# Kernel tuning notes

Measured on AMD Instinct MI355X. Metric: run time of the kernel, lower is better.

## Reference

```python
import jax, jax.numpy as jnp
import numpy as np

B, D = 8192, 1024          # batch, input dim
UNITS = [1024, 512]        # expert MLP hidden sizes
T, E_T, E_S = 2, 2, 4      # num_tasks, experts per task, shared experts
E = T * E_T + E_S          # total experts = 8


def setup_inputs() -> dict:
    key = jax.random.key(0)
    k = jax.random.split(key, 6)
    H, O = UNITS
    x = jax.random.normal(k[0], (B, D), dtype=jnp.float32)
    # glorot-normal-ish scaling for expert weights
    W1 = jax.random.normal(k[1], (E, D, H), dtype=jnp.float32) * np.sqrt(2.0 / (D + H))
    b1 = jnp.zeros((E, H), dtype=jnp.float32)
    W2 = jax.random.normal(k[2], (E, H, O), dtype=jnp.float32) * np.sqrt(2.0 / (H + O))
    b2 = jnp.zeros((E, O), dtype=jnp.float32)
    # per-task gate over (E_T + E_S) experts, no bias (use_bias=False in Dense)
    Wg = jax.random.normal(k[3], (T, D, E_T + E_S), dtype=jnp.float32) * np.sqrt(2.0 / (D + E_T + E_S))
    # shared gate over all E experts
    Wgs = jax.random.normal(k[4], (D, E), dtype=jnp.float32) * np.sqrt(2.0 / (D + E))
    return {"x": x, "W1": W1, "b1": b1, "W2": W2, "b2": b2, "Wg": Wg, "Wgs": Wgs}


def reference(x, W1, b1, W2, b2, Wg, Wgs):
    # All experts see the same input (2D-input path of CGC3: tf.tile over experts).
    # Batched grouped GEMM over the expert axis instead of a Python loop.
    h = jax.nn.relu(jnp.einsum('bd,edh->ebh', x, W1) + b1[:, None, :])   # [E,B,H]
    eo = jax.nn.relu(jnp.einsum('ebh,eho->ebo', h, W2) + b2[:, None, :]) # [E,B,O]

    outs = []
    for i in range(T):
        # experts for task i = its own E_T experts + the last E_S shared experts
        idx = jnp.array(list(range(i * E_T, (i + 1) * E_T)) + list(range(E - E_S, E)))
        g = jax.nn.softmax(x @ Wg[i], axis=-1)            # [B, E_T+E_S]
        sel = eo[idx]                                     # [E_T+E_S, B, O]
        outs.append(jnp.einsum('be,ebo->bo', g, sel))     # [B, O]
    # output_share=True: share tower gated over all experts
    gs = jax.nn.softmax(x @ Wgs, axis=-1)                 # [B, E]
    outs.append(jnp.einsum('be,ebo->bo', gs, eo))         # [B, O]
    return jnp.stack(outs, axis=1)                        # [B, T+1, O]
```

## Files before the change

kernel.cpp:

```cpp
#include <hip/hip_runtime.h>
#include <hip/hip_bf16.h>
#include <stdint.h>

#define B_SZ 8192
#define D_SZ 1024
#define H_SZ 1024
#define O_SZ 512
#define E_SZ 8

typedef float f32x4 __attribute__((ext_vector_type(4)));
typedef __bf16 bf16x8 __attribute__((ext_vector_type(8)));

typedef __attribute__((address_space(1))) uint32_t gu32;
typedef __attribute__((address_space(3))) uint32_t lu32;

__device__ __forceinline__ unsigned short f2bf(float f) {
    union { __hip_bfloat16 h; unsigned short u; } c;
    c.h = __float2bfloat16(f);
    return c.u;
}
__device__ __forceinline__ float bf2f(unsigned short u) {
    union { float f; uint32_t u; } c;
    c.u = ((uint32_t)u) << 16;
    return c.f;
}

__global__ __launch_bounds__(256) void k_convert_gates(const float* __restrict__ x,
                                                       const float* __restrict__ Wg,
                                                       const float* __restrict__ Wgs,
                                                       unsigned short* __restrict__ x_bf,
                                                       float* __restrict__ g_all) {
    const int wv = threadIdx.x >> 6;
    const int lane = threadIdx.x & 63;
    const int b = blockIdx.x * 4 + wv;
    const float* xr = x + (size_t)b * D_SZ;
    unsigned short* xo = x_bf + (size_t)b * D_SZ;
    float acc[20];
#pragma unroll
    for (int j = 0; j < 20; ++j) acc[j] = 0.f;
#pragma unroll 4
    for (int it = 0; it < 16; ++it) {
        const int d = it * 64 + lane;
        const float xv = xr[d];
        xo[d] = f2bf(xv);
        const float* w0 = Wg + (size_t)d * 6;
        const float* w1 = Wg + (size_t)D_SZ * 6 + (size_t)d * 6;
        const float* ws = Wgs + (size_t)d * 8;
#pragma unroll
        for (int j = 0; j < 6; ++j) acc[j] += xv * w0[j];
#pragma unroll
        for (int j = 0; j < 6; ++j) acc[6 + j] += xv * w1[j];
#pragma unroll
        for (int j = 0; j < 8; ++j) acc[12 + j] += xv * ws[j];
    }
#pragma unroll
    for (int j = 0; j < 20; ++j) {
        float v = acc[j];
#pragma unroll
        for (int s = 32; s > 0; s >>= 1) v += __shfl_down(v, s, 64);
        acc[j] = v;
    }
    if (lane == 0) {
        float* g = g_all + (size_t)b * 20;
#pragma unroll
        for (int t = 0; t < 3; ++t) {
            int base = (t == 0) ? 0 : (t == 1 ? 6 : 12);
            int cnt  = (t == 2) ? 8 : 6;
            float m = -1e30f;
            for (int j = 0; j < cnt; ++j) m = fmaxf(m, acc[base + j]);
            float ex[8]; float sum = 0.f;
            for (int j = 0; j < cnt; ++j) { ex[j] = __expf(acc[base + j] - m); sum += ex[j]; }
            float inv = 1.f / sum;
            for (int j = 0; j < cnt; ++j) g[base + j] = ex[j] * inv;
        }
    }
}

__global__ __launch_bounds__(512) void k_transpose_convert(const float* __restrict__ in,
                                                           unsigned short* __restrict__ out,
                                                           int R, int C) {
    __shared__ float tile[64][65];
    const float* src = in + (size_t)blockIdx.z * R * C;
    unsigned short* dst = out + (size_t)blockIdx.z * R * C;
    int c0 = blockIdx.x * 64, r0 = blockIdx.y * 64;
    int tx = threadIdx.x, ty = threadIdx.y;
#pragma unroll
    for (int rr = ty; rr < 64; rr += 8)
        tile[rr][tx] = src[(size_t)(r0 + rr) * C + c0 + tx];
    __syncthreads();
#pragma unroll
    for (int rr = ty; rr < 64; rr += 8)
        dst[(size_t)(c0 + rr) * R + r0 + tx] = f2bf(tile[tx][rr]);
}

__global__ __launch_bounds__(512, 2) void k_gemm8p(
    const unsigned short* __restrict__ A,
    const unsigned short* __restrict__ Bt,
    const float* __restrict__ bias,
    unsigned short* __restrict__ C,
    int M, int N, int K,
    long long sA, long long sB, long long sBias, long long sC, int e_base) {

    const int tid = threadIdx.x;
    const int lane = tid & 63, wid = tid >> 6;
    const int wr = wid >> 2, wc = wid & 3;
    const int lr = lane & 15, lg = lane >> 4;

    const int nwg = gridDim.x;
    const int wg = blockIdx.x;
    const int swz = (wg & 7) * (nwg >> 3) + (wg >> 3);
    const int nx = N >> 8;
    const int my = M >> 8;
    const int bx = swz % nx;
    const int t1 = swz / nx;
    const int by = t1 % my;
    const int e  = t1 / my + e_base;

    A    += (size_t)((long long)e * sA);
    Bt   += (size_t)((long long)e * sB);
    bias += (size_t)((long long)e * sBias);
    C    += (size_t)((long long)e * sC);

    const int m0 = by * 256, n0 = bx * 256;

    __shared__ __align__(16) unsigned short lds[65536];
    char* ldsb = (char*)lds;

    const int srow = tid >> 2;
    const int scol = (((tid & 3) ^ ((tid >> 3) & 3)) * 8);
    const int sdst = tid * 16;

    auto stageA2 = [&](int t) {
        const int bb = (t & 3) * 32768;
        const unsigned short* s0 = A + (size_t)(m0 + srow) * K + (t << 5) + scol;
        __builtin_amdgcn_global_load_lds((gu32*)s0, (lu32*)(ldsb + bb + sdst), 16, 0, 0);
        __builtin_amdgcn_global_load_lds((gu32*)(s0 + (size_t)128 * K),
                                         (lu32*)(ldsb + bb + 8192 + sdst), 16, 0, 0);
    };
    auto stageB2 = [&](int t) {
        const int bb = (t & 3) * 32768 + 16384;
        const unsigned short* s0 = Bt + (size_t)(n0 + srow) * K + (t << 5) + scol;
        __builtin_amdgcn_global_load_lds((gu32*)s0, (lu32*)(ldsb + bb + sdst), 16, 0, 0);
        __builtin_amdgcn_global_load_lds((gu32*)(s0 + (size_t)128 * K),
                                         (lu32*)(ldsb + bb + 8192 + sdst), 16, 0, 0);
    };

    const int cblk = (lg ^ ((lr >> 1) & 3)) * 16;
    const int aoff = wr * 8192 + lr * 64 + cblk;
    const int boff = 16384 + (wc >> 1) * 8192 + (wc & 1) * 4096 + lr * 64 + cblk;

    f32x4 acc[8][4];
#pragma unroll
    for (int i = 0; i < 8; ++i)
#pragma unroll
        for (int j = 0; j < 4; ++j)
            acc[i][j] = f32x4{0.f, 0.f, 0.f, 0.f};

    const int NT = K >> 5;

    stageA2(0); stageB2(0); stageA2(1); stageB2(1); stageA2(2); stageB2(2);
    asm volatile("s_waitcnt vmcnt(8)" ::: "memory");
    asm volatile("s_barrier" ::: "memory");

    for (int t = 0; t < NT; ++t) {
        const int bb = (t & 3) * 32768;
        const bool st = (t + 3 < NT);
        bf16x8 fa[4], fb[4];

#pragma unroll
        for (int i = 0; i < 4; ++i)
            fa[i] = *(const bf16x8*)(ldsb + bb + aoff + i * 1024);
#pragma unroll
        for (int j = 0; j < 4; ++j)
            fb[j] = *(const bf16x8*)(ldsb + bb + boff + j * 1024);
        if (st) stageA2(t + 3);
        asm volatile("s_barrier" ::: "memory");
        __builtin_amdgcn_s_setprio(1);
#pragma unroll
        for (int i = 0; i < 4; ++i)
#pragma unroll
            for (int j = 0; j < 4; ++j)
                acc[i][j] = __builtin_amdgcn_mfma_f32_16x16x32_bf16(fa[i], fb[j], acc[i][j], 0, 0, 0);
        __builtin_amdgcn_s_setprio(0);
        asm volatile("s_barrier" ::: "memory");

        bf16x8 ga[4];
#pragma unroll
        for (int i = 0; i < 4; ++i)
            ga[i] = *(const bf16x8*)(ldsb + bb + aoff + (4 + i) * 1024);
        if (st) stageB2(t + 3);
        asm volatile("s_barrier" ::: "memory");
        __builtin_amdgcn_s_setprio(1);
#pragma unroll
        for (int i = 0; i < 4; ++i)
#pragma unroll
            for (int j = 0; j < 4; ++j)
                acc[4 + i][j] = __builtin_amdgcn_mfma_f32_16x16x32_bf16(ga[i], fb[j], acc[4 + i][j], 0, 0, 0);
        __builtin_amdgcn_s_setprio(0);
        if (t < NT - 3)       { asm volatile("s_waitcnt vmcnt(8)" ::: "memory"); }
        else if (t == NT - 3) { asm volatile("s_waitcnt vmcnt(4)" ::: "memory"); }
        else if (t == NT - 2) { asm volatile("s_waitcnt vmcnt(0)" ::: "memory"); }
        asm volatile("s_barrier" ::: "memory");
    }

    unsigned short* ct = (unsigned short*)ldsb;
#pragma unroll
    for (int j = 0; j < 4; ++j) {
        const int nn = wc * 64 + j * 16 + lr;
        const float bv = bias[n0 + nn];
#pragma unroll
        for (int i = 0; i < 8; ++i) {
            const int mb = wr * 128 + i * 16 + lg * 4;
#pragma unroll
            for (int r = 0; r < 4; ++r) {
                float v = fmaxf(acc[i][j][r] + bv, 0.f);
                ct[(size_t)(mb + r) * 256 + nn] = f2bf(v);
            }
        }
    }
    __syncthreads();
#pragma unroll
    for (int it = 0; it < 16; ++it) {
        const int row = it * 16 + (tid >> 5);
        const int colE = (tid & 31) * 8;
        *(int4*)(&C[(size_t)(m0 + row) * N + n0 + colE]) =
            *(const int4*)(ldsb + it * 8192 + (size_t)tid * 16);
    }
}

__global__ __launch_bounds__(256) void k_combine(const unsigned short* __restrict__ eo,
                                                 const float* __restrict__ g_all,
                                                 float* __restrict__ out) {
    int idx4 = blockIdx.x * 256 + threadIdx.x;
    int b = idx4 >> 7;
    int o4 = (idx4 & 127) * 4;
    const float* g = g_all + (size_t)b * 20;
    float v[E_SZ][4];
#pragma unroll
    for (int e = 0; e < E_SZ; ++e) {
        ushort4 u = *(const ushort4*)(eo + (size_t)e * B_SZ * O_SZ + (size_t)b * O_SZ + o4);
        v[e][0] = bf2f(u.x); v[e][1] = bf2f(u.y); v[e][2] = bf2f(u.z); v[e][3] = bf2f(u.w);
    }
    float4 r0, r1, r2;
    float* p0 = (float*)&r0; float* p1 = (float*)&r1; float* p2 = (float*)&r2;
#pragma unroll
    for (int c = 0; c < 4; ++c) {
        p0[c] = g[0] * v[0][c] + g[1] * v[1][c] + g[2] * v[4][c] + g[3] * v[5][c]
              + g[4] * v[6][c] + g[5] * v[7][c];
        p1[c] = g[6] * v[2][c] + g[7] * v[3][c] + g[8] * v[4][c] + g[9] * v[5][c]
              + g[10] * v[6][c] + g[11] * v[7][c];
        float s = 0.f;
#pragma unroll
        for (int e = 0; e < E_SZ; ++e) s += g[12 + e] * v[e][c];
        p2[c] = s;
    }
    size_t ob = (size_t)b * (3 * O_SZ) + o4;
    *(float4*)(out + ob) = r0;
    *(float4*)(out + ob + O_SZ) = r1;
    *(float4*)(out + ob + 2 * O_SZ) = r2;
}

extern "C" void kernel_launch(void* const* d_in, const int* in_sizes, int n_in,
                              void* d_out, int out_size, void* d_ws, size_t ws_size,
                              hipStream_t stream) {
    const float* x   = (const float*)d_in[0];
    const float* W1  = (const float*)d_in[1];
    const float* b1  = (const float*)d_in[2];
    const float* W2  = (const float*)d_in[3];
    const float* b2  = (const float*)d_in[4];
    const float* Wg  = (const float*)d_in[5];
    const float* Wgs = (const float*)d_in[6];
    float* out = (float*)d_out;

    char* ws = (char*)d_ws;
    const size_t SZ_XBF  = (size_t)B_SZ * D_SZ * 2;
    const size_t SZ_W1T  = (size_t)E_SZ * H_SZ * D_SZ * 2;
    const size_t SZ_W2T  = (size_t)E_SZ * O_SZ * H_SZ * 2;
    const size_t SZ_EO   = (size_t)E_SZ * B_SZ * O_SZ * 2;
    const size_t SZ_G    = (size_t)B_SZ * 20 * 4;
    const size_t SZ_HBIG = (size_t)E_SZ * B_SZ * H_SZ * 2;

    unsigned short* x_bf = (unsigned short*)ws;              ws += SZ_XBF;
    unsigned short* W1T  = (unsigned short*)ws;              ws += SZ_W1T;
    unsigned short* W2T  = (unsigned short*)ws;              ws += SZ_W2T;
    unsigned short* eo   = (unsigned short*)ws;              ws += SZ_EO;
    float* g_all         = (float*)ws;                       ws += SZ_G;
    unsigned short* h_buf = (unsigned short*)ws;

    const size_t fixed = SZ_XBF + SZ_W1T + SZ_W2T + SZ_EO + SZ_G;
    const bool big = ws_size >= fixed + SZ_HBIG;

    k_convert_gates<<<B_SZ / 4, 256, 0, stream>>>(x, Wg, Wgs, x_bf, g_all);
    dim3 tb(64, 8);
    k_transpose_convert<<<dim3(H_SZ / 64, D_SZ / 64, E_SZ), tb, 0, stream>>>(W1, W1T, D_SZ, H_SZ);
    k_transpose_convert<<<dim3(O_SZ / 64, H_SZ / 64, E_SZ), tb, 0, stream>>>(W2, W2T, H_SZ, O_SZ);

    if (big) {
        k_gemm8p<<<(H_SZ / 256) * (B_SZ / 256) * E_SZ, 512, 0, stream>>>(
            x_bf, W1T, b1, h_buf, B_SZ, H_SZ, D_SZ,
            0LL, (long long)H_SZ * D_SZ, (long long)H_SZ, (long long)B_SZ * H_SZ, 0);
        k_gemm8p<<<(O_SZ / 256) * (B_SZ / 256) * E_SZ, 512, 0, stream>>>(
            h_buf, W2T, b2, eo, B_SZ, O_SZ, H_SZ,
            (long long)B_SZ * H_SZ, (long long)O_SZ * H_SZ, (long long)O_SZ, (long long)B_SZ * O_SZ, 0);
    } else {
        for (int e = 0; e < E_SZ; ++e) {
            k_gemm8p<<<(H_SZ / 256) * (B_SZ / 256), 512, 0, stream>>>(
                x_bf, W1T, b1, h_buf, B_SZ, H_SZ, D_SZ,
                0LL, (long long)H_SZ * D_SZ, (long long)H_SZ, 0LL, e);
            k_gemm8p<<<(O_SZ / 256) * (B_SZ / 256), 512, 0, stream>>>(
                h_buf, W2T, b2, eo, B_SZ, O_SZ, H_SZ,
                0LL, (long long)O_SZ * H_SZ, (long long)O_SZ, (long long)B_SZ * O_SZ, e);
        }
    }

    k_combine<<<(B_SZ * O_SZ / 4) / 256, 256, 0, stream>>>(eo, g_all, out);
}
```

Before: 312.5 us.

## Software-pipeline LDS fragment loads across K-steps in the bf16 GEMM

Restructures the GEMM main loop to process two K-tiles per iteration and double-buffer register fragments. LDS reads for the next half-tile are issued before the MFMAs of the current one, and the waitcnt/barrier placement is reorganised. The goal is to hide LDS read latency behind matrix-core work. It costs extra VGPRs for the duplicate fragment sets, which could cause spilling under the 512x2 launch bound, and the hand-placed waitcnt counts must still match the staging order.

```diff
diff --git a/kernel.cpp b/kernel.cpp
--- a/kernel.cpp
+++ b/kernel.cpp
@@ -93,7 +93,7 @@
         dst[(size_t)(c0 + rr) * R + r0 + tx] = f2bf(tile[tx][rr]);
 }
 
-__global__ __launch_bounds__(512, 2) void k_gemm8p(
+__global__ __launch_bounds__(512, 2) void k_gemm_pipe(
     const unsigned short* __restrict__ A,
     const unsigned short* __restrict__ Bt,
     const float* __restrict__ bias,
@@ -156,53 +156,70 @@
         for (int j = 0; j < 4; ++j)
             acc[i][j] = f32x4{0.f, 0.f, 0.f, 0.f};
 
+    auto mfma16 = [&](const bf16x8 (&fa)[4], const bf16x8 (&fb)[4], int rbase) {
+        __builtin_amdgcn_s_setprio(1);
+#pragma unroll
+        for (int i = 0; i < 4; ++i)
+#pragma unroll
+            for (int j = 0; j < 4; ++j)
+                acc[rbase + i][j] = __builtin_amdgcn_mfma_f32_16x16x32_bf16(
+                    fa[i], fb[j], acc[rbase + i][j], 0, 0, 0);
+        __builtin_amdgcn_s_setprio(0);
+    };
+
     const int NT = K >> 5;
 
     stageA2(0); stageB2(0); stageA2(1); stageB2(1); stageA2(2); stageB2(2);
     asm volatile("s_waitcnt vmcnt(8)" ::: "memory");
     asm volatile("s_barrier" ::: "memory");
 
-    for (int t = 0; t < NT; ++t) {
-        const int bb = (t & 3) * 32768;
-        const bool st = (t + 3 < NT);
-        bf16x8 fa[4], fb[4];
-
-#pragma unroll
-        for (int i = 0; i < 4; ++i)
-            fa[i] = *(const bf16x8*)(ldsb + bb + aoff + i * 1024);
-#pragma unroll
-        for (int j = 0; j < 4; ++j)
-            fb[j] = *(const bf16x8*)(ldsb + bb + boff + j * 1024);
-        if (st) stageA2(t + 3);
+    bf16x8 aU0[4], aL0[4], b0[4], aU1[4], aL1[4], b1v[4];
+#pragma unroll
+    for (int i = 0; i < 4; ++i) aU0[i] = *(const bf16x8*)(ldsb + aoff + i * 1024);
+#pragma unroll
+    for (int j = 0; j < 4; ++j) b0[j]  = *(const bf16x8*)(ldsb + boff + j * 1024);
+
+    for (int t = 0; t < NT; t += 2) {
+        const int bb0 = (t & 3) * 32768;
+        const int bb1 = ((t + 1) & 3) * 32768;
+        const int bb2 = ((t + 2) & 3) * 32768;
+
+#pragma unroll
+        for (int i = 0; i < 4; ++i) aL0[i] = *(const bf16x8*)(ldsb + bb0 + aoff + (4 + i) * 1024);
+        if (t + 2 < NT) { asm volatile("s_waitcnt vmcnt(4)" ::: "memory"); }
+        else            { asm volatile("s_waitcnt vmcnt(0)" ::: "memory"); }
         asm volatile("s_barrier" ::: "memory");
-        __builtin_amdgcn_s_setprio(1);
-#pragma unroll
-        for (int i = 0; i < 4; ++i)
-#pragma unroll
-            for (int j = 0; j < 4; ++j)
-                acc[i][j] = __builtin_amdgcn_mfma_f32_16x16x32_bf16(fa[i], fb[j], acc[i][j], 0, 0, 0);
-        __builtin_amdgcn_s_setprio(0);
+        if (t + 3 < NT) stageA2(t + 3);
+        mfma16(aU0, b0, 0);
+
+#pragma unroll
+        for (int i = 0; i < 4; ++i) aU1[i] = *(const bf16x8*)(ldsb + bb1 + aoff + i * 1024);
+#pragma unroll
+        for (int j = 0; j < 4; ++j) b1v[j] = *(const bf16x8*)(ldsb + bb1 + boff + j * 1024);
         asm volatile("s_barrier" ::: "memory");
-
-        bf16x8 ga[4];
-#pragma unroll
-        for (int i = 0; i < 4; ++i)
-            ga[i] = *(const bf16x8*)(ldsb + bb + aoff + (4 + i) * 1024);
-        if (st) stageB2(t + 3);
+        if (t + 3 < NT) stageB2(t + 3);
+        mfma16(aL0, b0, 4);
+
+#pragma unroll
+        for (int i = 0; i < 4; ++i) aL1[i] = *(const bf16x8*)(ldsb + bb1 + aoff + (4 + i) * 1024);
+        if (t + 3 < NT) { asm volatile("s_waitcnt vmcnt(4)" ::: "memory"); }
+        else            { asm volatile("s_waitcnt vmcnt(0)" ::: "memory"); }
         asm volatile("s_barrier" ::: "memory");
-        __builtin_amdgcn_s_setprio(1);
-#pragma unroll
-        for (int i = 0; i < 4; ++i)
-#pragma unroll
-            for (int j = 0; j < 4; ++j)
-                acc[4 + i][j] = __builtin_amdgcn_mfma_f32_16x16x32_bf16(ga[i], fb[j], acc[4 + i][j], 0, 0, 0);
-        __builtin_amdgcn_s_setprio(0);
-        if (t < NT - 3)       { asm volatile("s_waitcnt vmcnt(8)" ::: "memory"); }
-        else if (t == NT - 3) { asm volatile("s_waitcnt vmcnt(4)" ::: "memory"); }
-        else if (t == NT - 2) { asm volatile("s_waitcnt vmcnt(0)" ::: "memory"); }
+        if (t + 4 < NT) stageA2(t + 4);
+        mfma16(aU1, b1v, 0);
+
+        if (t + 2 < NT) {
+#pragma unroll
+            for (int i = 0; i < 4; ++i) aU0[i] = *(const bf16x8*)(ldsb + bb2 + aoff + i * 1024);
+#pragma unroll
+            for (int j = 0; j < 4; ++j) b0[j]  = *(const bf16x8*)(ldsb + bb2 + boff + j * 1024);
+        }
         asm volatile("s_barrier" ::: "memory");
-    }
-
+        if (t + 4 < NT) stageB2(t + 4);
+        mfma16(aL1, b1v, 4);
+    }
+
+    __syncthreads();
     unsigned short* ct = (unsigned short*)ldsb;
 #pragma unroll
     for (int j = 0; j < 4; ++j) {
@@ -296,18 +313,18 @@
     k_transpose_convert<<<dim3(O_SZ / 64, H_SZ / 64, E_SZ), tb, 0, stream>>>(W2, W2T, H_SZ, O_SZ);
 
     if (big) {
-        k_gemm8p<<<(H_SZ / 256) * (B_SZ / 256) * E_SZ, 512, 0, stream>>>(
+        k_gemm_pipe<<<(H_SZ / 256) * (B_SZ / 256) * E_SZ, 512, 0, stream>>>(
             x_bf, W1T, b1, h_buf, B_SZ, H_SZ, D_SZ,
             0LL, (long long)H_SZ * D_SZ, (long long)H_SZ, (long long)B_SZ * H_SZ, 0);
-        k_gemm8p<<<(O_SZ / 256) * (B_SZ / 256) * E_SZ, 512, 0, stream>>>(
+        k_gemm_pipe<<<(O_SZ / 256) * (B_SZ / 256) * E_SZ, 512, 0, stream>>>(
             h_buf, W2T, b2, eo, B_SZ, O_SZ, H_SZ,
             (long long)B_SZ * H_SZ, (long long)O_SZ * H_SZ, (long long)O_SZ, (long long)B_SZ * O_SZ, 0);
     } else {
         for (int e = 0; e < E_SZ; ++e) {
-            k_gemm8p<<<(H_SZ / 256) * (B_SZ / 256), 512, 0, stream>>>(
+            k_gemm_pipe<<<(H_SZ / 256) * (B_SZ / 256), 512, 0, stream>>>(
                 x_bf, W1T, b1, h_buf, B_SZ, H_SZ, D_SZ,
                 0LL, (long long)H_SZ * D_SZ, (long long)H_SZ, 0LL, e);
-            k_gemm8p<<<(O_SZ / 256) * (B_SZ / 256), 512, 0, stream>>>(
+            k_gemm_pipe<<<(O_SZ / 256) * (B_SZ / 256), 512, 0, stream>>>(
                 h_buf, W2T, b2, eo, B_SZ, O_SZ, H_SZ,
                 0LL, (long long)O_SZ * H_SZ, (long long)O_SZ, (long long)B_SZ * O_SZ, e);
         }
```

After: 307.0 us. No clear change (-1.8%).
